# Performance work log

Hardware: AMD Instinct MI355X
Metric: run time of the kernel (lower is better)

## Reference

```python
import jax, jax.numpy as jnp
import numpy as np

CAPACITY_FACTOR = 1.2


def setup_inputs() -> dict:
    key = jax.random.key(0)
    k1, k2 = jax.random.split(key, 2)
    D, E = 1024, 64
    x = jax.random.normal(k1, (8, 4096, D), dtype=jnp.float32)
    # xavier-uniform-ish router weight, zero bias (as in __init__)
    limit = np.sqrt(6.0 / (D + E)).astype(np.float32)
    W = jax.random.uniform(k2, (E, D), dtype=jnp.float32, minval=-limit, maxval=limit)
    b = jnp.zeros((E,), dtype=jnp.float32)
    return {"x": x, "W": W, "b": b, "detach_inputs": 0}


def reference(x, W, b, detach_inputs):
    bsz, seqlen, D = x.shape
    E = W.shape[0]                      # num experts == max_steps
    N = bsz * seqlen                    # num tokens
    x_flat = x.reshape(N, D)
    if detach_inputs:
        x_flat = jax.lax.stop_gradient(x_flat)
    logits = x_flat @ W.T + b           # [N, E]

    # expert-choice capacity (static python ints)
    k = max(1, int(N / max(1, E) * CAPACITY_FACTOR))
    k = min(k, N)

    # per-expert top-k over tokens: [E, k]
    topk_vals, topk_idx = jax.lax.top_k(logits.T, k)
    cand_tok = topk_idx.reshape(-1)                       # [E*k] token ids
    cand_exp = jnp.repeat(jnp.arange(E, dtype=jnp.int32), k)  # [E*k]
    cand_val = topk_vals.reshape(-1)                      # [E*k]

    # scatter-amax: best candidate logit per token (torch scatter_reduce_ 'amax')
    best_val = jnp.full((N,), -jnp.inf, dtype=logits.dtype).at[cand_tok].max(cand_val)

    # candidates that achieve the per-token max; dedup -> one expert per token
    # (tie-break: smallest expert index, matching first-occurrence after sort)
    eq = cand_val == best_val[cand_tok]
    exp_cand = jnp.where(eq, cand_exp, E).astype(jnp.int32)
    token_exp = jnp.full((N,), E, dtype=jnp.int32).at[cand_tok].min(exp_cand)
    selected = token_exp < E                              # token was picked by some expert
    assigned_expert = jnp.where(selected, token_exp, -1)  # [N], -1 = unassigned

    # load-balance loss from per-expert counts (bincount of assigned experts)
    sel_f = selected.astype(logits.dtype)
    counts = jnp.zeros((E,), dtype=logits.dtype).at[jnp.where(selected, token_exp, 0)].add(sel_f)
    mean_load = counts.mean()
    load_balance_loss = ((counts - mean_load) ** 2).mean() / (mean_load + 1e-9)

    best_val_out = jnp.where(selected, best_val, jnp.zeros((), logits.dtype))
    return (best_val_out, assigned_expert, selected, load_balance_loss)
```

## Files before the change

### kernel.cpp

```cpp
#include <hip/hip_runtime.h>
#include <math.h>

typedef __attribute__((ext_vector_type(4))) double d4;

__device__ inline unsigned fkey(float f) {
  unsigned bits = __float_as_uint(f);
  return (bits & 0x80000000u) ? ~bits : (bits | 0x80000000u);
}

__global__ __launch_bounds__(1024, 8) void logits_fused_kernel(
    const float* __restrict__ x, const float* __restrict__ W,
    const float* __restrict__ bias, float* __restrict__ logits,
    float* __restrict__ logitsT, int N, int D) {
  __shared__ __attribute__((aligned(16))) double xbuf[2][64 * 33];
  __shared__ __attribute__((aligned(16))) double wbuf[2][64 * 33];
  __shared__ unsigned s_fl;

  const int tid = threadIdx.x;
  const int tok0 = blockIdx.x * 64;
  const int l = tid & 63;
  const int l15 = l & 15;
  const int lk = l >> 4;

  double* pA = &wbuf[0][0];
  double* pB = &wbuf[0][64];
  if (tid < 64) {
    pA[l15 * 4 + lk] = (double)(l15 * 4 + lk + 1);
    pB[lk * 16 + l15] = (double)(l15 * 7 + lk * 3 + 2);
  }
  __syncthreads();
  if (tid < 64) {
    double a = pA[l15 * 4 + lk];
    double b = pB[lk * 16 + l15];
    d4 pacc = (d4)0.0;
    pacc = __builtin_amdgcn_mfma_f64_16x16x4f64(a, b, pacc, 0, 0, 0);
    unsigned res = 4;
    for (int m = 3; m >= 0; --m) {
      bool ok = true;
#pragma unroll
      for (int i = 0; i < 4; ++i) {
        int tr_ = (m < 2) ? ((m == 0) ? 4 * lk + i : lk + 4 * i) : l15;
        int tc_ = (m < 2) ? l15 : ((m == 2) ? 4 * lk + i : lk + 4 * i);
        double ref = 0.0;
#pragma unroll
        for (int kk = 0; kk < 4; ++kk) ref += pA[tr_ * 4 + kk] * pB[kk * 16 + tc_];
        ok = ok && (pacc[i] == ref);
      }
      if (__all(ok)) res = (unsigned)m;
    }
    if (l == 0) s_fl = res;
  }
  __syncthreads();
  const unsigned fl = s_fl;
  __syncthreads();

  if (fl < 4u) {
    const int w = tid >> 6;
    const int rb = (w & 3) * 16;
    const int cb = (w >> 2) * 16;

    d4 acc = (d4)0.0;

    const int srow = (tid & 511) >> 3;
    const int sc = tid & 7;
    const bool isx = (tid < 512);
    const float* gsrc = isx ? (x + (size_t)(tok0 + srow) * D + sc * 4)
                            : (W + (size_t)srow * D + sc * 4);
    const int ldoff = srow * 33 + sc * 4;

    const int nch = D >> 5;
    const int xa0 = (rb + l15) * 33 + lk;
    const int ba0 = (cb + l15) * 33 + lk;

    float4 rg = *(const float4*)gsrc;
    {
      double* ld = (isx ? &xbuf[0][0] : &wbuf[0][0]) + ldoff;
      ld[0] = (double)rg.x; ld[1] = (double)rg.y;
      ld[2] = (double)rg.z; ld[3] = (double)rg.w;
    }
    if (nch > 1) rg = *(const float4*)(gsrc + 32);
    __syncthreads();

    for (int c = 0; c < nch; ++c) {
      const int cbuf = c & 1;
      const int nb = cbuf ^ 1;
      if (c + 1 < nch) {
        double* ld = (isx ? &xbuf[nb][0] : &wbuf[nb][0]) + ldoff;
        ld[0] = (double)rg.x; ld[1] = (double)rg.y;
        ld[2] = (double)rg.z; ld[3] = (double)rg.w;
        if (c + 2 < nch) rg = *(const float4*)(gsrc + (c + 2) * 32);
      }
      const double* xr = &xbuf[cbuf][0];
      const double* wr = &wbuf[cbuf][0];
#pragma unroll
      for (int s = 0; s < 8; ++s) {
        double a = xr[xa0 + 4 * s];
        double b = wr[ba0 + 4 * s];
        acc = __builtin_amdgcn_mfma_f64_16x16x4f64(a, b, acc, 0, 0, 0);
      }
      __syncthreads();
    }

    float* ls = (float*)&xbuf[0][0];
#pragma unroll
    for (int i = 0; i < 4; ++i) {
      int tr_, tc_;
      if (fl < 2u) { tc_ = l15; tr_ = (fl == 0u) ? 4 * lk + i : lk + 4 * i; }
      else         { tr_ = l15; tc_ = (fl == 2u) ? 4 * lk + i : lk + 4 * i; }
      int col = cb + tc_;
      ls[(rb + tr_) * 68 + col] = (float)(acc[i] + (double)bias[col]);
    }
    __syncthreads();
    {
      int row = tid >> 4, c4 = tid & 15;
      float4 v = {ls[row * 68 + c4 * 4 + 0], ls[row * 68 + c4 * 4 + 1],
                  ls[row * 68 + c4 * 4 + 2], ls[row * 68 + c4 * 4 + 3]};
      *(float4*)(logits + (size_t)(tok0 + row) * 64 + c4 * 4) = v;
    }
    {
      int e = tid >> 4, t4 = tid & 15;
      float4 v = {ls[(t4 * 4 + 0) * 68 + e], ls[(t4 * 4 + 1) * 68 + e],
                  ls[(t4 * 4 + 2) * 68 + e], ls[(t4 * 4 + 3) * 68 + e]};
      *(float4*)(logitsT + (size_t)e * N + tok0 + t4 * 4) = v;
    }
  } else {
    for (int o = tid; o < 64 * 64; o += 1024) {
      int row = o >> 6, col = o & 63;
      const float* xp = x + (size_t)(tok0 + row) * D;
      const float* wp = W + (size_t)col * D;
      double s = 0.0;
      for (int kk = 0; kk < D; ++kk)
        s = fma((double)xp[kk], (double)wp[kk], s);
      float v = (float)(s + (double)bias[col]);
      logits[(size_t)(tok0 + row) * 64 + col] = v;
      logitsT[(size_t)col * N + tok0 + row] = v;
    }
  }
}

template <int KPT4>
__global__ __launch_bounds__(1024) void select_kernel(
    const float* __restrict__ logitsT, unsigned* __restrict__ ukeys,
    int N, int k) {
  __shared__ unsigned hist[16][256];
  __shared__ unsigned s_prefix, s_rem;
  const int e = blockIdx.x;
  const int tid = threadIdx.x;
  const int wid = tid >> 6;

  const float4* src = (const float4*)(logitsT + (size_t)e * N);
  unsigned key[KPT4 > 0 ? KPT4 * 4 : 4];
  if (KPT4 > 0) {
#pragma unroll
    for (int i = 0; i < (KPT4 > 0 ? KPT4 : 1); ++i) {
      float4 v = src[tid + i * 1024];
      key[i * 4 + 0] = fkey(v.x);
      key[i * 4 + 1] = fkey(v.y);
      key[i * 4 + 2] = fkey(v.z);
      key[i * 4 + 3] = fkey(v.w);
    }
  }
  if (tid == 0) { s_prefix = 0u; s_rem = (unsigned)k; }

  for (int r = 0; r < 4; ++r) {
    const int shift = 24 - 8 * r;
    const unsigned maskhi = (r == 0) ? 0u : (0xFFFFFFFFu << (shift + 8));
#pragma unroll
    for (int z = 0; z < 4; ++z) ((unsigned*)hist)[z * 1024 + tid] = 0u;
    __syncthreads();
    const unsigned prefix = s_prefix;
    if (KPT4 > 0) {
#pragma unroll
      for (int i = 0; i < (KPT4 > 0 ? KPT4 * 4 : 1); ++i) {
        unsigned u = key[i];
        if ((u & maskhi) == prefix)
          atomicAdd(&hist[wid][(u >> shift) & 255u], 1u);
      }
    } else {
      for (int i = tid; i < (N >> 2); i += 1024) {
        float4 v = src[i];
        unsigned u0 = fkey(v.x), u1 = fkey(v.y), u2 = fkey(v.z), u3 = fkey(v.w);
        if ((u0 & maskhi) == prefix) atomicAdd(&hist[wid][(u0 >> shift) & 255u], 1u);
        if ((u1 & maskhi) == prefix) atomicAdd(&hist[wid][(u1 >> shift) & 255u], 1u);
        if ((u2 & maskhi) == prefix) atomicAdd(&hist[wid][(u2 >> shift) & 255u], 1u);
        if ((u3 & maskhi) == prefix) atomicAdd(&hist[wid][(u3 >> shift) & 255u], 1u);
      }
    }
    __syncthreads();
    if (tid < 64) {
      unsigned rem = s_rem;
      unsigned h0 = 0, h1 = 0, h2 = 0, h3 = 0;
#pragma unroll
      for (int w = 0; w < 16; ++w) {
        h0 += hist[w][tid * 4 + 0];
        h1 += hist[w][tid * 4 + 1];
        h2 += hist[w][tid * 4 + 2];
        h3 += hist[w][tid * 4 + 3];
      }
      unsigned c3 = h3, c2 = c3 + h2, c1 = c2 + h1, c0 = c1 + h0;
      unsigned cum = c0;
#pragma unroll
      for (int off = 1; off < 64; off <<= 1) {
        unsigned v = __shfl_down(cum, off);
        if (tid + off < 64) cum += v;
      }
      unsigned above = cum - c0;
      if (above < rem && rem <= cum) {
        int j; unsigned abv;
        if (above + c3 >= rem)      { j = 3; abv = above; }
        else if (above + c2 >= rem) { j = 2; abv = above + c3; }
        else if (above + c1 >= rem) { j = 1; abv = above + c2; }
        else                        { j = 0; abv = above + c1; }
        s_rem = rem - abv;
        s_prefix = prefix | ((unsigned)(tid * 4 + j) << shift);
      }
    }
    __syncthreads();
  }
  if (tid == 0) ukeys[e] = s_prefix;
}

__global__ __launch_bounds__(256) void assign_kernel(
    const float* __restrict__ logits, const unsigned* __restrict__ ukeys,
    float* __restrict__ out, int N) {
  const int lane = threadIdx.x & 63;
  const int token = blockIdx.x * 4 + (threadIdx.x >> 6);

  float v = logits[(size_t)token * 64 + lane];
  unsigned u = fkey(v);
  bool cand = (u >= ukeys[lane]);
  float cv = cand ? v : -INFINITY;
  float m = cv;
#pragma unroll
  for (int off = 32; off; off >>= 1) m = fmaxf(m, __shfl_xor(m, off));
  unsigned long long mask = __ballot(cand && (v == m));
  bool sel = (mask != 0ull);
  int minexp = sel ? (__ffsll((long long)mask) - 1) : -1;

  if (lane == 0) {
    out[token] = sel ? m : 0.0f;
    out[N + token] = (float)minexp;
    out[2 * N + token] = sel ? 1.0f : 0.0f;
  }
}

__global__ __launch_bounds__(1024) void count_loss_kernel(
    const float* __restrict__ assigned, float* __restrict__ out, int N) {
  __shared__ unsigned hist[16][64];
  const int tid = threadIdx.x;
  const int wid = tid >> 6;
  hist[wid][tid & 63] = 0u;
  __syncthreads();
  const float4* src = (const float4*)assigned;
  for (int i = tid; i < (N >> 2); i += 1024) {
    float4 v = src[i];
    int e0 = (int)v.x, e1 = (int)v.y, e2 = (int)v.z, e3 = (int)v.w;
    if (e0 >= 0) atomicAdd(&hist[wid][e0], 1u);
    if (e1 >= 0) atomicAdd(&hist[wid][e1], 1u);
    if (e2 >= 0) atomicAdd(&hist[wid][e2], 1u);
    if (e3 >= 0) atomicAdd(&hist[wid][e3], 1u);
  }
  __syncthreads();
  if (tid < 64) {
    unsigned c = 0;
#pragma unroll
    for (int w = 0; w < 16; ++w) c += hist[w][tid];
    double cd = (double)c;
    double s = cd;
#pragma unroll
    for (int off = 32; off; off >>= 1) s += __shfl_xor(s, off);
    double mean = s / 64.0;
    double d = cd - mean;
    d = d * d;
#pragma unroll
    for (int off = 32; off; off >>= 1) d += __shfl_xor(d, off);
    if (tid == 0) out[3 * (size_t)N] = (float)((d / 64.0) / (mean + 1e-9));
  }
}

extern "C" void kernel_launch(void* const* d_in, const int* in_sizes, int n_in,
                              void* d_out, int out_size, void* d_ws, size_t ws_size,
                              hipStream_t stream) {
  const float* x = (const float*)d_in[0];
  const float* W = (const float*)d_in[1];
  const float* b = (const float*)d_in[2];

  const int E = in_sizes[2];
  const int D = in_sizes[1] / E;
  const int N = in_sizes[0] / D;

  int k = (int)((double)N / (double)(E > 1 ? E : 1) * 1.2);
  if (k < 1) k = 1;
  if (k > N) k = N;

  const size_t NE = (size_t)N * E;
  float* out = (float*)d_out;

  float* logits = (float*)d_ws;
  float* logitsT = logits + NE;
  unsigned* ukeys = (unsigned*)(logitsT + NE);

  logits_fused_kernel<<<N / 64, 1024, 0, stream>>>(x, W, b, logits, logitsT,
                                                   N, D);
  if (N == 32768)
    select_kernel<8><<<64, 1024, 0, stream>>>(logitsT, ukeys, N, k);
  else
    select_kernel<0><<<64, 1024, 0, stream>>>(logitsT, ukeys, N, k);
  assign_kernel<<<N / 4, 256, 0, stream>>>(logits, ukeys, out, N);
  count_loss_kernel<<<1, 1024, 0, stream>>>(out + N, out, N);
}
```

Before: 110.5 us.

## Shrink logits GEMM block to four waves with four accumulator tiles each

Cuts the logits kernel from 1024 to 256 threads per block. Each wave now computes a 16x64 strip using four f64 MFMA accumulators, so one A fragment is reused across four B fragments, and each thread loads four float4s per chunk instead of one. This lowers the LDS read traffic per MFMA and the barrier cost per block, at the price of more registers per thread and fewer waves available to hide memory latency.

```diff
diff --git a/kernel.cpp b/kernel.cpp
--- a/kernel.cpp
+++ b/kernel.cpp
@@ -8,7 +8,14 @@
   return (bits & 0x80000000u) ? ~bits : (bits | 0x80000000u);
 }
 
-__global__ __launch_bounds__(1024, 8) void logits_fused_kernel(
+#define STORE4D(base, off, v)                          \
+  {                                                    \
+    double* _p = (base) + (off);                       \
+    _p[0] = (double)(v).x; _p[1] = (double)(v).y;      \
+    _p[2] = (double)(v).z; _p[3] = (double)(v).w;      \
+  }
+
+__global__ __launch_bounds__(256, 2) void logits_fused_kernel(
     const float* __restrict__ x, const float* __restrict__ W,
     const float* __restrict__ bias, float* __restrict__ logits,
     float* __restrict__ logitsT, int N, int D) {
@@ -56,75 +63,105 @@
 
   if (fl < 4u) {
     const int w = tid >> 6;
-    const int rb = (w & 3) * 16;
-    const int cb = (w >> 2) * 16;
-
-    d4 acc = (d4)0.0;
-
-    const int srow = (tid & 511) >> 3;
+    const int rb = w * 16;
+
+    d4 acc[4];
+#pragma unroll
+    for (int ct = 0; ct < 4; ++ct) acc[ct] = (d4)0.0;
+
+    const int srow = tid >> 3;
     const int sc = tid & 7;
-    const bool isx = (tid < 512);
-    const float* gsrc = isx ? (x + (size_t)(tok0 + srow) * D + sc * 4)
-                            : (W + (size_t)srow * D + sc * 4);
-    const int ldoff = srow * 33 + sc * 4;
+    const float* g0 = x + (size_t)(tok0 + srow) * D + sc * 4;
+    const float* g1 = x + (size_t)(tok0 + 32 + srow) * D + sc * 4;
+    const float* g2 = W + (size_t)srow * D + sc * 4;
+    const float* g3 = W + (size_t)(32 + srow) * D + sc * 4;
+    const int lo0 = srow * 33 + sc * 4;
+    const int lo1 = (32 + srow) * 33 + sc * 4;
 
     const int nch = D >> 5;
     const int xa0 = (rb + l15) * 33 + lk;
-    const int ba0 = (cb + l15) * 33 + lk;
-
-    float4 rg = *(const float4*)gsrc;
-    {
-      double* ld = (isx ? &xbuf[0][0] : &wbuf[0][0]) + ldoff;
-      ld[0] = (double)rg.x; ld[1] = (double)rg.y;
-      ld[2] = (double)rg.z; ld[3] = (double)rg.w;
-    }
-    if (nch > 1) rg = *(const float4*)(gsrc + 32);
+    const int ba0 = l15 * 33 + lk;
+
+    float4 r0 = *(const float4*)g0;
+    float4 r1 = *(const float4*)g1;
+    float4 r2 = *(const float4*)g2;
+    float4 r3 = *(const float4*)g3;
+    STORE4D(&xbuf[0][0], lo0, r0);
+    STORE4D(&xbuf[0][0], lo1, r1);
+    STORE4D(&wbuf[0][0], lo0, r2);
+    STORE4D(&wbuf[0][0], lo1, r3);
+    if (nch > 1) {
+      r0 = *(const float4*)(g0 + 32);
+      r1 = *(const float4*)(g1 + 32);
+      r2 = *(const float4*)(g2 + 32);
+      r3 = *(const float4*)(g3 + 32);
+    }
     __syncthreads();
 
     for (int c = 0; c < nch; ++c) {
       const int cbuf = c & 1;
       const int nb = cbuf ^ 1;
       if (c + 1 < nch) {
-        double* ld = (isx ? &xbuf[nb][0] : &wbuf[nb][0]) + ldoff;
-        ld[0] = (double)rg.x; ld[1] = (double)rg.y;
-        ld[2] = (double)rg.z; ld[3] = (double)rg.w;
-        if (c + 2 < nch) rg = *(const float4*)(gsrc + (c + 2) * 32);
+        STORE4D(&xbuf[nb][0], lo0, r0);
+        STORE4D(&xbuf[nb][0], lo1, r1);
+        STORE4D(&wbuf[nb][0], lo0, r2);
+        STORE4D(&wbuf[nb][0], lo1, r3);
+        if (c + 2 < nch) {
+          const int kc = (c + 2) * 32;
+          r0 = *(const float4*)(g0 + kc);
+          r1 = *(const float4*)(g1 + kc);
+          r2 = *(const float4*)(g2 + kc);
+          r3 = *(const float4*)(g3 + kc);
+        }
       }
       const double* xr = &xbuf[cbuf][0];
       const double* wr = &wbuf[cbuf][0];
 #pragma unroll
       for (int s = 0; s < 8; ++s) {
         double a = xr[xa0 + 4 * s];
-        double b = wr[ba0 + 4 * s];
-        acc = __builtin_amdgcn_mfma_f64_16x16x4f64(a, b, acc, 0, 0, 0);
+        double b0 = wr[ba0 + 0 * 16 * 33 + 4 * s];
+        double b1 = wr[ba0 + 1 * 16 * 33 + 4 * s];
+        double b2 = wr[ba0 + 2 * 16 * 33 + 4 * s];
+        double b3 = wr[ba0 + 3 * 16 * 33 + 4 * s];
+        acc[0] = __builtin_amdgcn_mfma_f64_16x16x4f64(a, b0, acc[0], 0, 0, 0);
+        acc[1] = __builtin_amdgcn_mfma_f64_16x16x4f64(a, b1, acc[1], 0, 0, 0);
+        acc[2] = __builtin_amdgcn_mfma_f64_16x16x4f64(a, b2, acc[2], 0, 0, 0);
+        acc[3] = __builtin_amdgcn_mfma_f64_16x16x4f64(a, b3, acc[3], 0, 0, 0);
       }
       __syncthreads();
     }
 
     float* ls = (float*)&xbuf[0][0];
 #pragma unroll
-    for (int i = 0; i < 4; ++i) {
-      int tr_, tc_;
-      if (fl < 2u) { tc_ = l15; tr_ = (fl == 0u) ? 4 * lk + i : lk + 4 * i; }
-      else         { tr_ = l15; tc_ = (fl == 2u) ? 4 * lk + i : lk + 4 * i; }
-      int col = cb + tc_;
-      ls[(rb + tr_) * 68 + col] = (float)(acc[i] + (double)bias[col]);
-    }
-    __syncthreads();
-    {
-      int row = tid >> 4, c4 = tid & 15;
+    for (int ct = 0; ct < 4; ++ct) {
+#pragma unroll
+      for (int i = 0; i < 4; ++i) {
+        int tr_, tc_;
+        if (fl < 2u) { tc_ = l15; tr_ = (fl == 0u) ? 4 * lk + i : lk + 4 * i; }
+        else         { tr_ = l15; tc_ = (fl == 2u) ? 4 * lk + i : lk + 4 * i; }
+        int col = ct * 16 + tc_;
+        ls[(rb + tr_) * 68 + col] = (float)(acc[ct][i] + (double)bias[col]);
+      }
+    }
+    __syncthreads();
+#pragma unroll
+    for (int it = 0; it < 4; ++it) {
+      int slot = it * 256 + tid;
+      int row = slot >> 4, c4 = slot & 15;
       float4 v = {ls[row * 68 + c4 * 4 + 0], ls[row * 68 + c4 * 4 + 1],
                   ls[row * 68 + c4 * 4 + 2], ls[row * 68 + c4 * 4 + 3]};
       *(float4*)(logits + (size_t)(tok0 + row) * 64 + c4 * 4) = v;
     }
-    {
-      int e = tid >> 4, t4 = tid & 15;
+#pragma unroll
+    for (int it = 0; it < 4; ++it) {
+      int slot = it * 256 + tid;
+      int e = slot >> 4, t4 = slot & 15;
       float4 v = {ls[(t4 * 4 + 0) * 68 + e], ls[(t4 * 4 + 1) * 68 + e],
                   ls[(t4 * 4 + 2) * 68 + e], ls[(t4 * 4 + 3) * 68 + e]};
       *(float4*)(logitsT + (size_t)e * N + tok0 + t4 * 4) = v;
     }
   } else {
-    for (int o = tid; o < 64 * 64; o += 1024) {
+    for (int o = tid; o < 64 * 64; o += 256) {
       int row = o >> 6, col = o & 63;
       const float* xp = x + (size_t)(tok0 + row) * D;
       const float* wp = W + (size_t)col * D;
@@ -300,8 +337,8 @@
   float* logitsT = logits + NE;
   unsigned* ukeys = (unsigned*)(logitsT + NE);
 
-  logits_fused_kernel<<<N / 64, 1024, 0, stream>>>(x, W, b, logits, logitsT,
-                                                   N, D);
+  logits_fused_kernel<<<N / 64, 256, 0, stream>>>(x, W, b, logits, logitsT,
+                                                  N, D);
   if (N == 32768)
     select_kernel<8><<<64, 1024, 0, stream>>>(logitsT, ukeys, N, k);
   else
```

After: 116.4 us. 5.3% more time.

## Halve logits block to 512 threads with two MFMA tiles per wave

Applied to the files above, without the earlier changes.

The logits GEMM kernel now runs with 512 threads per block instead of 1024. Each wave computes two 16x16 output tiles that share the same A fragment, so each loaded x value feeds two MFMAs, and every thread stages both an x and a W float4 per chunk. All LDS operands are loaded into registers before the MFMA chain, which raises register use per thread but lowers LDS reads per MFMA and halves the barrier participants. The launch bounds change to (512,4), and the epilogue and fallback loops are adjusted to cover the tile with half as many threads.

```diff
diff --git a/kernel.cpp b/kernel.cpp
--- a/kernel.cpp
+++ b/kernel.cpp
@@ -8,7 +8,14 @@
   return (bits & 0x80000000u) ? ~bits : (bits | 0x80000000u);
 }
 
-__global__ __launch_bounds__(1024, 8) void logits_fused_kernel(
+#define STORE4D(base, off, v)                          \
+  {                                                    \
+    double* _p = (base) + (off);                       \
+    _p[0] = (double)(v).x; _p[1] = (double)(v).y;      \
+    _p[2] = (double)(v).z; _p[3] = (double)(v).w;      \
+  }
+
+__global__ __launch_bounds__(512, 4) void logits_fused_kernel(
     const float* __restrict__ x, const float* __restrict__ W,
     const float* __restrict__ bias, float* __restrict__ logits,
     float* __restrict__ logitsT, int N, int D) {
@@ -57,74 +64,91 @@
   if (fl < 4u) {
     const int w = tid >> 6;
     const int rb = (w & 3) * 16;
-    const int cb = (w >> 2) * 16;
-
-    d4 acc = (d4)0.0;
-
-    const int srow = (tid & 511) >> 3;
+    const int cb = (w >> 2) * 32;
+
+    d4 acc0 = (d4)0.0;
+    d4 acc1 = (d4)0.0;
+
+    const int srow = tid >> 3;
     const int sc = tid & 7;
-    const bool isx = (tid < 512);
-    const float* gsrc = isx ? (x + (size_t)(tok0 + srow) * D + sc * 4)
-                            : (W + (size_t)srow * D + sc * 4);
-    const int ldoff = srow * 33 + sc * 4;
+    const float* gx = x + (size_t)(tok0 + srow) * D + sc * 4;
+    const float* gw = W + (size_t)srow * D + sc * 4;
+    const int lo = srow * 33 + sc * 4;
 
     const int nch = D >> 5;
     const int xa0 = (rb + l15) * 33 + lk;
     const int ba0 = (cb + l15) * 33 + lk;
 
-    float4 rg = *(const float4*)gsrc;
-    {
-      double* ld = (isx ? &xbuf[0][0] : &wbuf[0][0]) + ldoff;
-      ld[0] = (double)rg.x; ld[1] = (double)rg.y;
-      ld[2] = (double)rg.z; ld[3] = (double)rg.w;
-    }
-    if (nch > 1) rg = *(const float4*)(gsrc + 32);
+    float4 rx = *(const float4*)gx;
+    float4 rw = *(const float4*)gw;
+    STORE4D(&xbuf[0][0], lo, rx);
+    STORE4D(&wbuf[0][0], lo, rw);
+    if (nch > 1) {
+      rx = *(const float4*)(gx + 32);
+      rw = *(const float4*)(gw + 32);
+    }
     __syncthreads();
 
     for (int c = 0; c < nch; ++c) {
       const int cbuf = c & 1;
       const int nb = cbuf ^ 1;
       if (c + 1 < nch) {
-        double* ld = (isx ? &xbuf[nb][0] : &wbuf[nb][0]) + ldoff;
-        ld[0] = (double)rg.x; ld[1] = (double)rg.y;
-        ld[2] = (double)rg.z; ld[3] = (double)rg.w;
-        if (c + 2 < nch) rg = *(const float4*)(gsrc + (c + 2) * 32);
+        STORE4D(&xbuf[nb][0], lo, rx);
+        STORE4D(&wbuf[nb][0], lo, rw);
+        if (c + 2 < nch) {
+          rx = *(const float4*)(gx + (c + 2) * 32);
+          rw = *(const float4*)(gw + (c + 2) * 32);
+        }
       }
       const double* xr = &xbuf[cbuf][0];
       const double* wr = &wbuf[cbuf][0];
+      double a[8], b0[8], b1[8];
 #pragma unroll
       for (int s = 0; s < 8; ++s) {
-        double a = xr[xa0 + 4 * s];
-        double b = wr[ba0 + 4 * s];
-        acc = __builtin_amdgcn_mfma_f64_16x16x4f64(a, b, acc, 0, 0, 0);
+        a[s]  = xr[xa0 + 4 * s];
+        b0[s] = wr[ba0 + 4 * s];
+        b1[s] = wr[ba0 + 16 * 33 + 4 * s];
+      }
+#pragma unroll
+      for (int s = 0; s < 8; ++s) {
+        acc0 = __builtin_amdgcn_mfma_f64_16x16x4f64(a[s], b0[s], acc0, 0, 0, 0);
+        acc1 = __builtin_amdgcn_mfma_f64_16x16x4f64(a[s], b1[s], acc1, 0, 0, 0);
       }
       __syncthreads();
     }
 
     float* ls = (float*)&xbuf[0][0];
 #pragma unroll
-    for (int i = 0; i < 4; ++i) {
-      int tr_, tc_;
-      if (fl < 2u) { tc_ = l15; tr_ = (fl == 0u) ? 4 * lk + i : lk + 4 * i; }
-      else         { tr_ = l15; tc_ = (fl == 2u) ? 4 * lk + i : lk + 4 * i; }
-      int col = cb + tc_;
-      ls[(rb + tr_) * 68 + col] = (float)(acc[i] + (double)bias[col]);
-    }
-    __syncthreads();
-    {
-      int row = tid >> 4, c4 = tid & 15;
+    for (int ct = 0; ct < 2; ++ct) {
+      const d4* ac = (ct == 0) ? &acc0 : &acc1;
+#pragma unroll
+      for (int i = 0; i < 4; ++i) {
+        int tr_, tc_;
+        if (fl < 2u) { tc_ = l15; tr_ = (fl == 0u) ? 4 * lk + i : lk + 4 * i; }
+        else         { tr_ = l15; tc_ = (fl == 2u) ? 4 * lk + i : lk + 4 * i; }
+        int col = cb + ct * 16 + tc_;
+        ls[(rb + tr_) * 68 + col] = (float)((*ac)[i] + (double)bias[col]);
+      }
+    }
+    __syncthreads();
+#pragma unroll
+    for (int it = 0; it < 2; ++it) {
+      int slot = it * 512 + tid;
+      int row = slot >> 4, c4 = slot & 15;
       float4 v = {ls[row * 68 + c4 * 4 + 0], ls[row * 68 + c4 * 4 + 1],
                   ls[row * 68 + c4 * 4 + 2], ls[row * 68 + c4 * 4 + 3]};
       *(float4*)(logits + (size_t)(tok0 + row) * 64 + c4 * 4) = v;
     }
-    {
-      int e = tid >> 4, t4 = tid & 15;
+#pragma unroll
+    for (int it = 0; it < 2; ++it) {
+      int slot = it * 512 + tid;
+      int e = slot >> 4, t4 = slot & 15;
       float4 v = {ls[(t4 * 4 + 0) * 68 + e], ls[(t4 * 4 + 1) * 68 + e],
                   ls[(t4 * 4 + 2) * 68 + e], ls[(t4 * 4 + 3) * 68 + e]};
       *(float4*)(logitsT + (size_t)e * N + tok0 + t4 * 4) = v;
     }
   } else {
-    for (int o = tid; o < 64 * 64; o += 1024) {
+    for (int o = tid; o < 64 * 64; o += 512) {
       int row = o >> 6, col = o & 63;
       const float* xp = x + (size_t)(tok0 + row) * D;
       const float* wp = W + (size_t)col * D;
@@ -300,8 +324,8 @@
   float* logitsT = logits + NE;
   unsigned* ukeys = (unsigned*)(logitsT + NE);
 
-  logits_fused_kernel<<<N / 64, 1024, 0, stream>>>(x, W, b, logits, logitsT,
-                                                   N, D);
+  logits_fused_kernel<<<N / 64, 512, 0, stream>>>(x, W, b, logits, logitsT,
+                                                  N, D);
   if (N == 32768)
     select_kernel<8><<<64, 1024, 0, stream>>>(logitsT, ukeys, N, k);
   else
```

Result: no change. 111.8 us (+1.1%).
